# Performance work log

Measured on AMD Instinct MI355X. Metric: run time of the kernel, lower is better.

Reference implementation:

```python
import jax, jax.numpy as jnp
import numpy as np

BLOCK = 16
NVFP4_LEVELS = jnp.array([0.0, 0.5, 1.0, 1.5, 2.0, 3.0, 4.0, 6.0], dtype=jnp.float32)


def _quantize_to_nvfp4(x_blocks):
    # x_blocks: [n_blocks, BLOCK]
    amax = jnp.clip(jnp.max(jnp.abs(x_blocks), axis=-1, keepdims=True), 1e-12, None)
    scale = amax / 6.0
    x_norm = jnp.abs(x_blocks) / scale
    idx = jnp.argmin(jnp.abs(x_norm[..., None] - NVFP4_LEVELS), axis=-1)
    return jnp.sign(x_blocks) * NVFP4_LEVELS[idx] * scale


def setup_inputs() -> dict:
    key = jax.random.key(0)
    k1, k2, k3, k4 = jax.random.split(key, 4)
    B, S, H, O = 16, 1024, 1152, 4608
    x = jax.random.normal(k1, (B, S, H), dtype=jnp.float32)
    w_quantized = jax.random.normal(k2, (O, H), dtype=jnp.float32) * 0.02
    smooth_scale = jax.random.uniform(k3, (H,), dtype=jnp.float32, minval=0.5, maxval=2.0)
    bias = jax.random.normal(k4, (O,), dtype=jnp.float32) * 0.02
    return {"x": x, "w_quantized": w_quantized, "smooth_scale": smooth_scale, "bias": bias}


def reference(x, w_quantized, smooth_scale, bias):
    orig_shape = x.shape
    H = orig_shape[-1]
    # SmoothQuant activation prescale
    x_s = (x * smooth_scale).reshape(-1, H)              # [T, H]
    # per-token prescale to [-6, 6]
    token_max = jnp.clip(jnp.max(jnp.abs(x_s), axis=-1, keepdims=True), 1e-12, None)
    pre_scale = token_max / 6.0
    x_pre = x_s / pre_scale
    # blockwise NVFP4 fake quant
    x_q = _quantize_to_nvfp4(x_pre.reshape(-1, BLOCK)).reshape(x_s.shape)
    x_q = x_q * pre_scale                                # restore token scale
    out = x_q.reshape(orig_shape) @ w_quantized.T + bias  # F.linear
    return out
```

## Files before the change

kernel.cpp:

```cpp
#include <hip/hip_runtime.h>
#include <hip/hip_bf16.h>

typedef __attribute__((ext_vector_type(8))) _Float16 f16x8;
typedef __attribute__((ext_vector_type(4))) float  f32x4;

#define H_DIM 1152
#define H_VEC (H_DIM / 4)

__device__ __forceinline__ float nvfp4_level(float xn) {
    return xn <= 0.25f ? 0.0f
         : xn <= 0.75f ? 0.5f
         : xn <= 1.25f ? 1.0f
         : xn <= 1.75f ? 1.5f
         : xn <= 2.5f  ? 2.0f
         : xn <= 3.5f  ? 3.0f
         : xn <= 5.0f  ? 4.0f : 6.0f;
}

__global__ __launch_bounds__(64) void quant_kernel(
    const float4* __restrict__ x4, const float4* __restrict__ s4,
    _Float16* __restrict__ xq)
{
    const int t    = blockIdx.x;
    const int lane = threadIdx.x;
    const float4* xrow = x4 + (size_t)t * H_VEC;

    float4 v[5];
    int    fidx[5];
    float  m = 0.f;
    #pragma unroll
    for (int i = 0; i < 5; ++i) {
        const int f = (i < 4) ? (lane + 64 * i) : (256 + (lane & 31));
        fidx[i] = f;
        const float4 xx = xrow[f];
        const float4 ss = s4[f];
        float4 vv;
        vv.x = xx.x * ss.x; vv.y = xx.y * ss.y;
        vv.z = xx.z * ss.z; vv.w = xx.w * ss.w;
        v[i] = vv;
        m = fmaxf(m, fmaxf(fmaxf(fabsf(vv.x), fabsf(vv.y)),
                           fmaxf(fabsf(vv.z), fabsf(vv.w))));
    }
    #pragma unroll
    for (int off = 32; off; off >>= 1)
        m = fmaxf(m, __shfl_xor(m, off, 64));
    const float pre_scale = fmaxf(m, 1e-12f) / 6.0f;

    #pragma unroll
    for (int i = 0; i < 5; ++i) {
        float4 p;
        p.x = v[i].x / pre_scale;
        p.y = v[i].y / pre_scale;
        p.z = v[i].z / pre_scale;
        p.w = v[i].w / pre_scale;
        float g = fmaxf(fmaxf(fabsf(p.x), fabsf(p.y)),
                        fmaxf(fabsf(p.z), fabsf(p.w)));
        g = fmaxf(g, __shfl_xor(g, 1, 64));
        g = fmaxf(g, __shfl_xor(g, 2, 64));
        const float scale = fmaxf(g, 1e-12f) / 6.0f;

        alignas(8) _Float16 o[4];
        {
            float q;
            q = copysignf(nvfp4_level(fabsf(p.x) / scale) * scale, p.x) * pre_scale;
            o[0] = (_Float16)q;
            q = copysignf(nvfp4_level(fabsf(p.y) / scale) * scale, p.y) * pre_scale;
            o[1] = (_Float16)q;
            q = copysignf(nvfp4_level(fabsf(p.z) / scale) * scale, p.z) * pre_scale;
            o[2] = (_Float16)q;
            q = copysignf(nvfp4_level(fabsf(p.w) / scale) * scale, p.w) * pre_scale;
            o[3] = (_Float16)q;
        }
        if (i < 4 || lane < 32) {
            _Float16* dst = xq + (size_t)t * H_DIM + fidx[i] * 4;
            *(uint2*)dst = *(const uint2*)o;
        }
    }
}

__global__ __launch_bounds__(256) void wconv_kernel(
    const float* __restrict__ w, _Float16* __restrict__ wq, int n)
{
    int i = (blockIdx.x * 256 + threadIdx.x) * 4;
    if (i < n) {
        float4 v = *(const float4*)(w + i);
        alignas(8) _Float16 o[4];
        o[0] = (_Float16)v.x;
        o[1] = (_Float16)v.y;
        o[2] = (_Float16)v.z;
        o[3] = (_Float16)v.w;
        *(uint2*)(wq + i) = *(const uint2*)o;
    }
}

__device__ __forceinline__ void async_copy16(const void* gptr, void* lptr)
{
    __builtin_amdgcn_global_load_lds(
        (const __attribute__((address_space(1))) unsigned int*)gptr,
        (__attribute__((address_space(3))) unsigned int*)lptr,
        16, 0, 0);
}

__global__ __launch_bounds__(256) void gemm_bt_kernel(
    const _Float16* __restrict__ A,
    const _Float16* __restrict__ B,
    const float* __restrict__ bias,
    float* __restrict__ C,
    int M, int N, int K)
{
    __shared__ _Float16 sA[128 * 32];
    __shared__ _Float16 sB[128 * 32];

    const int tid  = threadIdx.x;
    const int wave = tid >> 6;
    const int lane = tid & 63;
    const int m0 = blockIdx.y * 128;
    const int n0 = blockIdx.x * 128;
    const int wave_m = (wave & 1) * 64;
    const int wave_n = (wave >> 1) * 64;
    const int lane16 = lane & 15;
    const int quad   = lane >> 4;

    const int rowA = lane >> 2;
    const int colA = (lane & 3) * 8;

    f32x4 acc[4][4] = {};

    for (int k0 = 0; k0 < K; k0 += 32) {
        __syncthreads();
        #pragma unroll
        for (int s = 0; s < 2; ++s) {
            const int R = wave * 32 + s * 16;
            async_copy16(A + (size_t)(m0 + R + rowA) * K + k0 + colA, sA + R * 32);
            async_copy16(B + (size_t)(n0 + R + rowA) * K + k0 + colA, sB + R * 32);
        }
        __syncthreads();

        f16x8 a[4], b[4];
        #pragma unroll
        for (int i = 0; i < 4; ++i)
            a[i] = *(const f16x8*)(sA + (wave_m + i * 16 + lane16) * 32 + quad * 8);
        #pragma unroll
        for (int j = 0; j < 4; ++j)
            b[j] = *(const f16x8*)(sB + (wave_n + j * 16 + lane16) * 32 + quad * 8);
        #pragma unroll
        for (int i = 0; i < 4; ++i)
            #pragma unroll
            for (int j = 0; j < 4; ++j)
                acc[i][j] = __builtin_amdgcn_mfma_f32_16x16x32_f16(a[i], b[j], acc[i][j], 0, 0, 0);
    }

    #pragma unroll
    for (int i = 0; i < 4; ++i) {
        const int m = m0 + wave_m + i * 16 + quad * 4;
        #pragma unroll
        for (int j = 0; j < 4; ++j) {
            const int n = n0 + wave_n + j * 16 + lane16;
            const float bv = bias[n];
            float* cp = C + (size_t)m * N + n;
            #pragma unroll
            for (int r = 0; r < 4; ++r)
                cp[(size_t)r * N] = acc[i][j][r] + bv;
        }
    }
}

extern "C" void kernel_launch(void* const* d_in, const int* in_sizes, int n_in,
                              void* d_out, int out_size, void* d_ws, size_t ws_size,
                              hipStream_t stream)
{
    const float* x      = (const float*)d_in[0];
    const float* w      = (const float*)d_in[1];
    const float* smooth = (const float*)d_in[2];
    const float* bias   = (const float*)d_in[3];
    float* out = (float*)d_out;

    const int H = in_sizes[2];
    const int T = in_sizes[0] / H;
    const int O = in_sizes[3];

    _Float16* xq = (_Float16*)d_ws;
    _Float16* wq = (_Float16*)((char*)d_ws + (size_t)T * H * sizeof(_Float16));

    quant_kernel<<<T, 64, 0, stream>>>((const float4*)x, (const float4*)smooth, xq);
    wconv_kernel<<<(O * H / 4 + 255) / 256, 256, 0, stream>>>(w, wq, O * H);

    dim3 grid(O / 128, T / 128);
    gemm_bt_kernel<<<grid, 256, 0, stream>>>(xq, wq, bias, out, T, O, H);
}
```

Before: 569.4 us.

## Rewrite GEMM with 256x256x64 double-buffered swizzled LDS tiles and grid remap

The GEMM moves from 128x128x32 tiles with single-buffered loads to 256x256x64 tiles computed by 8 waves. Global-to-LDS async loads are double-buffered and overlap with MFMA work, and an XOR swizzle on the LDS layout avoids bank conflicts. The workgroup index is remapped to improve L2 locality, and MFMA sections run at raised wave priority. The quant kernel now packs four tokens per 256-thread block. The cost is higher register and LDS pressure: each block uses 128KB of LDS, which may limit occupancy.

```diff
diff --git a/kernel.cpp b/kernel.cpp
--- a/kernel.cpp
+++ b/kernel.cpp
@@ -17,12 +17,12 @@
          : xn <= 5.0f  ? 4.0f : 6.0f;
 }
 
-__global__ __launch_bounds__(64) void quant_kernel(
+__global__ __launch_bounds__(256) void quant_kernel(
     const float4* __restrict__ x4, const float4* __restrict__ s4,
     _Float16* __restrict__ xq)
 {
-    const int t    = blockIdx.x;
-    const int lane = threadIdx.x;
+    const int t    = (blockIdx.x << 2) + (threadIdx.x >> 6);
+    const int lane = threadIdx.x & 63;
     const float4* xrow = x4 + (size_t)t * H_VEC;
 
     float4 v[5];
@@ -101,66 +101,135 @@
         16, 0, 0);
 }
 
-__global__ __launch_bounds__(256) void gemm_bt_kernel(
+#define BARRIER() do { asm volatile("" ::: "memory"); \
+                       __builtin_amdgcn_s_barrier();  \
+                       asm volatile("" ::: "memory"); } while (0)
+
+#define BM 256
+#define BN 256
+#define BK 64
+
+__global__ __launch_bounds__(512, 2) void gemm_bt_kernel(
     const _Float16* __restrict__ A,
     const _Float16* __restrict__ B,
     const float* __restrict__ bias,
     float* __restrict__ C,
     int M, int N, int K)
 {
-    __shared__ _Float16 sA[128 * 32];
-    __shared__ _Float16 sB[128 * 32];
-
-    const int tid  = threadIdx.x;
-    const int wave = tid >> 6;
-    const int lane = tid & 63;
-    const int m0 = blockIdx.y * 128;
-    const int n0 = blockIdx.x * 128;
-    const int wave_m = (wave & 1) * 64;
-    const int wave_n = (wave >> 1) * 64;
+    __shared__ alignas(16) _Float16 sA[2][BM * BK];
+    __shared__ alignas(16) _Float16 sB[2][BN * BK];
+
+    const int tid    = threadIdx.x;
+    const int wave   = tid >> 6;
+    const int lane   = tid & 63;
     const int lane16 = lane & 15;
     const int quad   = lane >> 4;
 
-    const int rowA = lane >> 2;
-    const int colA = (lane & 3) * 8;
-
-    f32x4 acc[4][4] = {};
-
-    for (int k0 = 0; k0 < K; k0 += 32) {
-        __syncthreads();
+    const int nbx = gridDim.x;
+    const int nwg = nbx * gridDim.y;
+    int bid = blockIdx.y * nbx + blockIdx.x;
+    if ((nwg & 7) == 0) {
+        const int cpx = nwg >> 3;
+        bid = (bid & 7) * cpx + (bid >> 3);
+    }
+    const int m0 = (bid / nbx) * BM;
+    const int n0 = (bid % nbx) * BN;
+
+    const int wr = wave >> 2;
+    const int wc = wave & 3;
+
+    const int NT = K / BK;
+
+    int srcA[4], srcB[4], ldst[4];
+    #pragma unroll
+    for (int s = 0; s < 4; ++s) {
+        const int base = (wave * 4 + s) * 64;
+        const int c    = base + lane;
+        const int r    = c >> 3;
+        const int sw   = ((c & 7) * 8) ^ ((r & 7) << 3);
+        srcA[s] = (m0 + r) * K + sw;
+        srcB[s] = (n0 + r) * K + sw;
+        ldst[s] = base * 16;
+    }
+
+    auto stage = [&](int t, int d) {
+        const int k0 = t * BK;
         #pragma unroll
-        for (int s = 0; s < 2; ++s) {
-            const int R = wave * 32 + s * 16;
-            async_copy16(A + (size_t)(m0 + R + rowA) * K + k0 + colA, sA + R * 32);
-            async_copy16(B + (size_t)(n0 + R + rowA) * K + k0 + colA, sB + R * 32);
-        }
-        __syncthreads();
-
-        f16x8 a[4], b[4];
+        for (int s = 0; s < 4; ++s) {
+            async_copy16(A + srcA[s] + k0, (char*)(&sA[d][0]) + ldst[s]);
+            async_copy16(B + srcB[s] + k0, (char*)(&sB[d][0]) + ldst[s]);
+        }
+    };
+
+    stage(0, 0);
+    if (NT > 1) stage(1, 1);
+    asm volatile("s_waitcnt vmcnt(8)" ::: "memory");
+    BARRIER();
+
+    f32x4 acc[8][4] = {};
+    f16x8 b[4][2];
+
+    for (int t = 0; t < NT; ++t) {
+        const int d = t & 1;
+        const _Float16* tA = &sA[d][0];
+        const _Float16* tB = &sB[d][0];
+
         #pragma unroll
-        for (int i = 0; i < 4; ++i)
-            a[i] = *(const f16x8*)(sA + (wave_m + i * 16 + lane16) * 32 + quad * 8);
-        #pragma unroll
-        for (int j = 0; j < 4; ++j)
-            b[j] = *(const f16x8*)(sB + (wave_n + j * 16 + lane16) * 32 + quad * 8);
-        #pragma unroll
-        for (int i = 0; i < 4; ++i)
+        for (int p = 0; p < 4; ++p) {
+            f16x8 a[2][2];
             #pragma unroll
-            for (int j = 0; j < 4; ++j)
-                acc[i][j] = __builtin_amdgcn_mfma_f32_16x16x32_f16(a[i], b[j], acc[i][j], 0, 0, 0);
-    }
-
-    #pragma unroll
-    for (int i = 0; i < 4; ++i) {
-        const int m = m0 + wave_m + i * 16 + quad * 4;
+            for (int ii = 0; ii < 2; ++ii) {
+                const int r = wr * 128 + (p * 2 + ii) * 16 + lane16;
+                #pragma unroll
+                for (int ks = 0; ks < 2; ++ks)
+                    a[ii][ks] = *(const f16x8*)(tA + r * 64 +
+                                 ((ks * 32 + quad * 8) ^ ((r & 7) << 3)));
+            }
+            if (p == 0) {
+                #pragma unroll
+                for (int j = 0; j < 4; ++j) {
+                    const int rb = wc * 64 + j * 16 + lane16;
+                    #pragma unroll
+                    for (int ks = 0; ks < 2; ++ks)
+                        b[j][ks] = *(const f16x8*)(tB + rb * 64 +
+                                    ((ks * 32 + quad * 8) ^ ((rb & 7) << 3)));
+                }
+            }
+            BARRIER();
+            asm volatile("s_waitcnt lgkmcnt(0)" ::: "memory");
+            __builtin_amdgcn_s_setprio(1);
+            #pragma unroll
+            for (int ii = 0; ii < 2; ++ii)
+                #pragma unroll
+                for (int j = 0; j < 4; ++j)
+                    #pragma unroll
+                    for (int ks = 0; ks < 2; ++ks)
+                        acc[p * 2 + ii][j] = __builtin_amdgcn_mfma_f32_16x16x32_f16(
+                            a[ii][ks], b[j][ks], acc[p * 2 + ii][j], 0, 0, 0);
+            __builtin_amdgcn_s_setprio(0);
+            BARRIER();
+        }
+
+        if (t + 2 < NT) {
+            stage(t + 2, d);
+            asm volatile("s_waitcnt vmcnt(8)" ::: "memory");
+        } else {
+            asm volatile("s_waitcnt vmcnt(0)" ::: "memory");
+        }
+        BARRIER();
+    }
+
+    #pragma unroll
+    for (int i = 0; i < 8; ++i) {
+        const int m = m0 + wr * 128 + i * 16 + quad * 4;
         #pragma unroll
         for (int j = 0; j < 4; ++j) {
-            const int n = n0 + wave_n + j * 16 + lane16;
+            const int n = n0 + wc * 64 + j * 16 + lane16;
             const float bv = bias[n];
             float* cp = C + (size_t)m * N + n;
             #pragma unroll
-            for (int r = 0; r < 4; ++r)
-                cp[(size_t)r * N] = acc[i][j][r] + bv;
+            for (int r2 = 0; r2 < 4; ++r2)
+                cp[(size_t)r2 * N] = acc[i][j][r2] + bv;
         }
     }
 }
@@ -182,9 +251,9 @@
     _Float16* xq = (_Float16*)d_ws;
     _Float16* wq = (_Float16*)((char*)d_ws + (size_t)T * H * sizeof(_Float16));
 
-    quant_kernel<<<T, 64, 0, stream>>>((const float4*)x, (const float4*)smooth, xq);
+    quant_kernel<<<T / 4, 256, 0, stream>>>((const float4*)x, (const float4*)smooth, xq);
     wconv_kernel<<<(O * H / 4 + 255) / 256, 256, 0, stream>>>(w, wq, O * H);
 
-    dim3 grid(O / 128, T / 128);
-    gemm_bt_kernel<<<grid, 256, 0, stream>>>(xq, wq, bias, out, T, O, H);
-}
+    dim3 grid(O / BN, T / BM);
+    gemm_bt_kernel<<<grid, 512, 0, stream>>>(xq, wq, bias, out, T, O, H);
+}
```

New measurement: 576.3 us. No clear change (+1.2%).
